# Kernel tuning notes

Hardware: AMD Instinct MI355X
Metric: run time of the kernel (lower is better)

Reference implementation:

```python
import jax, jax.numpy as jnp
import numpy as np

N = 50000   # nodes
E = 800000  # edges (before self-loops)
IN, HID, OUT = 128, 128, 64


def gcn_norm(edge_index, num_nodes):
    # add self loops with weight 1, then symmetric deg^-1/2 normalization
    loop = jnp.arange(num_nodes, dtype=edge_index.dtype)
    row = jnp.concatenate([edge_index[0], loop])
    col = jnp.concatenate([edge_index[1], loop])
    ew = jnp.ones(row.shape[0], dtype=jnp.float32)
    deg = jax.ops.segment_sum(ew, col, num_segments=num_nodes)
    dis = jnp.where(deg > 0, jax.lax.rsqrt(deg), 0.0)
    norm = dis[row] * ew * dis[col]
    return row, col, norm


def gcn_conv(x, row, col, norm, W, b):
    h = x @ W                                   # [N, F_out] dense GEMM
    msg = h[row] * norm[:, None]                # gather + scale over edges
    out = jax.ops.segment_sum(msg, col, num_segments=x.shape[0])  # scatter-add
    return out + b


def setup_inputs() -> dict:
    key = jax.random.key(0)
    k0, k1, k2, k3, k4, k5 = jax.random.split(key, 6)
    x = jax.random.normal(k0, (N, IN), dtype=jnp.float32)
    edge_index = jax.random.randint(k1, (2, E), 0, N, dtype=jnp.int32)
    # glorot-style init for linear weights, zeros for bias (PyG default)
    W1 = jax.random.normal(k2, (IN, HID), dtype=jnp.float32) * np.float32(np.sqrt(1.0 / IN))
    b1 = jnp.zeros((HID,), dtype=jnp.float32)
    W2 = jax.random.normal(k3, (HID, OUT), dtype=jnp.float32) * np.float32(np.sqrt(1.0 / HID))
    b2 = jnp.zeros((OUT,), dtype=jnp.float32)
    return {"x": x, "edge_index": edge_index, "W1": W1, "b1": b1, "W2": W2, "b2": b2}


def reference(x, edge_index, W1, b1, W2, b2):
    row, col, norm = gcn_norm(edge_index, x.shape[0])
    h = jax.nn.relu(gcn_conv(x, row, col, norm, W1, b1))
    # dropout is a no-op in eval mode (training=False)
    out = gcn_conv(h, row, col, norm, W2, b2)
    return out
```

## Files before the change

### kernel.cpp

```cpp
#include <hip/hip_runtime.h>
#include <hip/hip_fp16.h>


#define Nn 50000
#define Ne 800000
#define SCAN_B ((Nn + 1023) / 1024)

using f16x8 = _Float16 __attribute__((ext_vector_type(8)));
using f32x4 = float __attribute__((ext_vector_type(4)));

__global__ __launch_bounds__(256) void k_count(const int* __restrict__ col,
                                               int* __restrict__ degi,
                                               unsigned short* __restrict__ rank) {
  int e = blockIdx.x * 256 + threadIdx.x;
  if (e < Ne) rank[e] = (unsigned short)atomicAdd(&degi[col[e]], 1);
}

__global__ __launch_bounds__(1024) void k_scan1(const int* __restrict__ degi,
                                                int* __restrict__ rowptr,
                                                float* __restrict__ dis,
                                                int* __restrict__ bsum) {
  __shared__ int wsum[16];
  int tid = threadIdx.x;
  int lane = tid & 63, wid = tid >> 6;
  int i = blockIdx.x * 1024 + tid;
  int v = (i < Nn) ? degi[i] : 0;
  if (i < Nn) dis[i] = rsqrtf((float)(v + 1));
  int incl = v;
  #pragma unroll
  for (int off = 1; off < 64; off <<= 1) {
    int t = __shfl_up(incl, off);
    if (lane >= off) incl += t;
  }
  if (lane == 63) wsum[wid] = incl;
  __syncthreads();
  if (wid == 0) {
    int wv = (lane < 16) ? wsum[lane] : 0;
    #pragma unroll
    for (int off = 1; off < 16; off <<= 1) {
      int t = __shfl_up(wv, off);
      if (lane >= off) wv += t;
    }
    if (lane < 16) wsum[lane] = wv;
  }
  __syncthreads();
  int woff = (wid > 0) ? wsum[wid - 1] : 0;
  if (i < Nn) rowptr[i] = woff + incl - v;
  if (tid == 0) bsum[blockIdx.x] = wsum[15];
}

__global__ __launch_bounds__(1024) void k_scan3(int* __restrict__ rowptr,
                                                const int* __restrict__ bsum) {
  __shared__ int off_s;
  int tid = threadIdx.x;
  if (tid < 64) {
    int v = (tid < SCAN_B) ? bsum[tid] : 0;
    int incl = v;
    #pragma unroll
    for (int off = 1; off < 64; off <<= 1) {
      int t = __shfl_up(incl, off);
      if (tid >= off) incl += t;
    }
    if (tid == (int)blockIdx.x) off_s = incl - v;
    if (blockIdx.x == 0 && tid == SCAN_B - 1) rowptr[Nn] = incl;
  }
  __syncthreads();
  int i = blockIdx.x * 1024 + tid;
  if (i < Nn) rowptr[i] += off_s;
}

__global__ __launch_bounds__(256) void k_fill(const int* __restrict__ row,
                                              const int* __restrict__ col,
                                              const int* __restrict__ rowptr,
                                              const unsigned short* __restrict__ rank,
                                              unsigned short* __restrict__ csr) {
  int e = blockIdx.x * 256 + threadIdx.x;
  if (e >= Ne) return;
  int r = row[e], c = col[e];
  csr[rowptr[c] + (int)rank[e]] = (unsigned short)r;
}

template <int LDO>
__global__ __launch_bounds__(256) void k_gemm_mfma(const float* __restrict__ X,
                                                   const float* __restrict__ W,
                                                   __half* __restrict__ H, int n) {
  __shared__ _Float16 Xs[64 * 136];
  __shared__ _Float16 Wts[LDO * 136];
  const int tid = threadIdx.x;
  const int base = blockIdx.x * 64;

  {
    constexpr int C4 = LDO / 4;
    for (int idx4 = tid; idx4 < 32 * LDO; idx4 += 256) {
      int k = idx4 / C4;
      int c = (idx4 % C4) * 4;
      float4 wv = ((const float4*)W)[idx4];
      Wts[(c + 0) * 136 + k] = (_Float16)wv.x;
      Wts[(c + 1) * 136 + k] = (_Float16)wv.y;
      Wts[(c + 2) * 136 + k] = (_Float16)wv.z;
      Wts[(c + 3) * 136 + k] = (_Float16)wv.w;
    }
  }
  {
    for (int u = tid; u < 64 * 16; u += 256) {
      int r = u >> 4, seg = u & 15;
      int node = base + r;
      if (node >= n) node = n - 1;
      const float4* xg = (const float4*)(X + (size_t)node * 128 + seg * 8);
      float4 x0 = xg[0], x1 = xg[1];
      f16x8 hv;
      hv[0] = (_Float16)x0.x; hv[1] = (_Float16)x0.y;
      hv[2] = (_Float16)x0.z; hv[3] = (_Float16)x0.w;
      hv[4] = (_Float16)x1.x; hv[5] = (_Float16)x1.y;
      hv[6] = (_Float16)x1.z; hv[7] = (_Float16)x1.w;
      *(f16x8*)&Xs[r * 136 + seg * 8] = hv;
    }
  }
  __syncthreads();

  const int w = tid >> 6, lane = tid & 63;
  const int quad = lane >> 4, mrow = lane & 15;
  constexpr int NCT = LDO / 16;

  f32x4 acc[NCT];
  #pragma unroll
  for (int ct = 0; ct < NCT; ++ct) acc[ct] = (f32x4){0.f, 0.f, 0.f, 0.f};

  #pragma unroll
  for (int ko = 0; ko < 4; ++ko) {
    f16x8 av = *(const f16x8*)&Xs[(w * 16 + mrow) * 136 + ko * 32 + quad * 8];
    #pragma unroll
    for (int ct = 0; ct < NCT; ++ct) {
      f16x8 bv = *(const f16x8*)&Wts[(ct * 16 + mrow) * 136 + ko * 32 + quad * 8];
      acc[ct] = __builtin_amdgcn_mfma_f32_16x16x32_f16(av, bv, acc[ct], 0, 0, 0);
    }
  }

  #pragma unroll
  for (int ct = 0; ct < NCT; ++ct) {
    #pragma unroll
    for (int r = 0; r < 4; ++r) {
      int node = base + w * 16 + quad * 4 + r;
      if (node < n)
        H[(size_t)node * LDO + ct * 16 + mrow] = __float2half(acc[ct][r]);
    }
  }
}

__device__ __forceinline__ float2 h2f(unsigned int u) {
  return __half22float2(*(const __half2*)&u);
}

__global__ __launch_bounds__(256) void k_agg128_gemm64(
    const __half* __restrict__ H, const unsigned short* __restrict__ csr,
    const int* __restrict__ rowptr, const float* __restrict__ dis,
    const float* __restrict__ bias, const float* __restrict__ W2,
    __half* __restrict__ H2, int n) {
  __shared__ _Float16 Wts[64 * 136];
  __shared__ _Float16 Hs[16 * 136];

  const int tid = threadIdx.x;
  const int wid = tid >> 6, lane = tid & 63;
  const int sub = lane >> 4, fl = lane & 15;
  const int nb = wid * 4 + sub;
  const int v = blockIdx.x * 16 + nb;

  for (int idx4 = tid; idx4 < 2048; idx4 += 256) {
    int k = idx4 >> 4;
    int c = (idx4 & 15) * 4;
    float4 wv = ((const float4*)W2)[idx4];
    Wts[(c + 0) * 136 + k] = (_Float16)wv.x;
    Wts[(c + 1) * 136 + k] = (_Float16)wv.y;
    Wts[(c + 2) * 136 + k] = (_Float16)wv.z;
    Wts[(c + 3) * 136 + k] = (_Float16)wv.w;
  }

  float a0 = 0, a1 = 0, a2 = 0, a3 = 0, a4 = 0, a5 = 0, a6 = 0, a7 = 0;
  float d = 0.f;
  if (v < n) {
    int s = rowptr[v], e = rowptr[v + 1];
    d = dis[v];
    float sw = d * d;
    const uint4* Hq = (const uint4*)H;
    uint4 hv = Hq[(size_t)v * 16 + fl];
    float2 p0 = h2f(hv.x), p1 = h2f(hv.y), p2 = h2f(hv.z), p3 = h2f(hv.w);
    a0 = p0.x * sw; a1 = p0.y * sw; a2 = p1.x * sw; a3 = p1.y * sw;
    a4 = p2.x * sw; a5 = p2.y * sw; a6 = p3.x * sw; a7 = p3.y * sw;
    constexpr int D = 6;
    int i = s;
    for (; i + D <= e; i += D) {
      int srcs[D];
      uint4 q[D];
      float wd[D];
      #pragma unroll
      for (int j = 0; j < D; ++j) srcs[j] = csr[i + j];
      #pragma unroll
      for (int j = 0; j < D; ++j) q[j] = Hq[(size_t)srcs[j] * 16 + fl];
      #pragma unroll
      for (int j = 0; j < D; ++j) wd[j] = dis[srcs[j]];
      #pragma unroll
      for (int j = 0; j < D; ++j) {
        float w = wd[j] * d;
        float2 t;
        t = h2f(q[j].x); a0 = fmaf(w, t.x, a0); a1 = fmaf(w, t.y, a1);
        t = h2f(q[j].y); a2 = fmaf(w, t.x, a2); a3 = fmaf(w, t.y, a3);
        t = h2f(q[j].z); a4 = fmaf(w, t.x, a4); a5 = fmaf(w, t.y, a5);
        t = h2f(q[j].w); a6 = fmaf(w, t.x, a6); a7 = fmaf(w, t.y, a7);
      }
    }
    if (i < e) {
      int srcs[D];
      uint4 q[D];
      float wd[D];
      #pragma unroll
      for (int j = 0; j < D; ++j) {
        int idx = (i + j < e) ? i + j : e - 1;
        srcs[j] = csr[idx];
      }
      #pragma unroll
      for (int j = 0; j < D; ++j) q[j] = Hq[(size_t)srcs[j] * 16 + fl];
      #pragma unroll
      for (int j = 0; j < D; ++j) wd[j] = dis[srcs[j]];
      #pragma unroll
      for (int j = 0; j < D; ++j) {
        float w = (i + j < e) ? wd[j] * d : 0.f;
        float2 t;
        t = h2f(q[j].x); a0 = fmaf(w, t.x, a0); a1 = fmaf(w, t.y, a1);
        t = h2f(q[j].y); a2 = fmaf(w, t.x, a2); a3 = fmaf(w, t.y, a3);
        t = h2f(q[j].z); a4 = fmaf(w, t.x, a4); a5 = fmaf(w, t.y, a5);
        t = h2f(q[j].w); a6 = fmaf(w, t.x, a6); a7 = fmaf(w, t.y, a7);
      }
    }
  }
  {
    const float4* Bq = (const float4*)bias;
    float4 b0 = Bq[fl * 2], b1v = Bq[fl * 2 + 1];
    f16x8 hrow;
    hrow[0] = (_Float16)fmaxf(a0 + b0.x, 0.f);
    hrow[1] = (_Float16)fmaxf(a1 + b0.y, 0.f);
    hrow[2] = (_Float16)fmaxf(a2 + b0.z, 0.f);
    hrow[3] = (_Float16)fmaxf(a3 + b0.w, 0.f);
    hrow[4] = (_Float16)fmaxf(a4 + b1v.x, 0.f);
    hrow[5] = (_Float16)fmaxf(a5 + b1v.y, 0.f);
    hrow[6] = (_Float16)fmaxf(a6 + b1v.z, 0.f);
    hrow[7] = (_Float16)fmaxf(a7 + b1v.w, 0.f);
    *(f16x8*)&Hs[nb * 136 + fl * 8] = hrow;
  }
  __syncthreads();

  const int quad = lane >> 4, mrow = lane & 15;
  f32x4 acc = (f32x4){0.f, 0.f, 0.f, 0.f};
  #pragma unroll
  for (int ko = 0; ko < 4; ++ko) {
    f16x8 av = *(const f16x8*)&Hs[mrow * 136 + ko * 32 + quad * 8];
    f16x8 bv = *(const f16x8*)&Wts[(wid * 16 + mrow) * 136 + ko * 32 + quad * 8];
    acc = __builtin_amdgcn_mfma_f32_16x16x32_f16(av, bv, acc, 0, 0, 0);
  }
  #pragma unroll
  for (int r = 0; r < 4; ++r) {
    int node = blockIdx.x * 16 + quad * 4 + r;
    if (node < n)
      H2[(size_t)node * 64 + wid * 16 + mrow] = __float2half(acc[r]);
  }
}

__global__ __launch_bounds__(256) void k_agg64(const __half* __restrict__ H,
                                               const unsigned short* __restrict__ csr,
                                               const int* __restrict__ rowptr,
                                               const float* __restrict__ dis,
                                               const float* __restrict__ bias,
                                               float* __restrict__ Out, int n) {
  const int wid = threadIdx.x >> 6, lane = threadIdx.x & 63;
  const int sub = lane >> 4, fl = lane & 15;
  int v = blockIdx.x * 16 + wid * 4 + sub;
  if (v >= n) return;
  int s = rowptr[v], e = rowptr[v + 1];
  float d = dis[v];
  float sw = d * d;
  const uint2* Hq = (const uint2*)H;
  uint2 hv = Hq[(size_t)v * 16 + fl];
  float2 p0 = h2f(hv.x), p1 = h2f(hv.y);
  float a0 = p0.x * sw, a1 = p0.y * sw, a2 = p1.x * sw, a3 = p1.y * sw;
  constexpr int D = 8;
  int i = s;
  for (; i + D <= e; i += D) {
    int srcs[D];
    uint2 q[D];
    float wd[D];
    #pragma unroll
    for (int j = 0; j < D; ++j) srcs[j] = csr[i + j];
    #pragma unroll
    for (int j = 0; j < D; ++j) q[j] = Hq[(size_t)srcs[j] * 16 + fl];
    #pragma unroll
    for (int j = 0; j < D; ++j) wd[j] = dis[srcs[j]];
    #pragma unroll
    for (int j = 0; j < D; ++j) {
      float w = wd[j] * d;
      float2 t;
      t = h2f(q[j].x); a0 = fmaf(w, t.x, a0); a1 = fmaf(w, t.y, a1);
      t = h2f(q[j].y); a2 = fmaf(w, t.x, a2); a3 = fmaf(w, t.y, a3);
    }
  }
  if (i < e) {
    int srcs[D];
    uint2 q[D];
    float wd[D];
    #pragma unroll
    for (int j = 0; j < D; ++j) {
      int idx = (i + j < e) ? i + j : e - 1;
      srcs[j] = csr[idx];
    }
    #pragma unroll
    for (int j = 0; j < D; ++j) q[j] = Hq[(size_t)srcs[j] * 16 + fl];
    #pragma unroll
    for (int j = 0; j < D; ++j) wd[j] = dis[srcs[j]];
    #pragma unroll
    for (int j = 0; j < D; ++j) {
      float w = (i + j < e) ? wd[j] * d : 0.f;
      float2 t;
      t = h2f(q[j].x); a0 = fmaf(w, t.x, a0); a1 = fmaf(w, t.y, a1);
      t = h2f(q[j].y); a2 = fmaf(w, t.x, a2); a3 = fmaf(w, t.y, a3);
    }
  }
  const float4* Bq = (const float4*)bias;
  float4 b = Bq[fl];
  float4 o = make_float4(a0 + b.x, a1 + b.y, a2 + b.z, a3 + b.w);
  ((float4*)(Out + (size_t)v * 64))[fl] = o;
}

extern "C" void kernel_launch(void* const* d_in, const int* in_sizes, int n_in,
                              void* d_out, int out_size, void* d_ws, size_t ws_size,
                              hipStream_t stream) {
  const float* x  = (const float*)d_in[0];
  const int*   ei = (const int*)d_in[1];
  const int*   row = ei;
  const int*   col = ei + Ne;
  const float* W1 = (const float*)d_in[2];
  const float* b1 = (const float*)d_in[3];
  const float* W2 = (const float*)d_in[4];
  const float* b2 = (const float*)d_in[5];
  float* out = (float*)d_out;

  char* ws = (char*)d_ws;
  size_t off = 0;
  auto alloc = [&](size_t bytes) -> void* {
    void* p = ws + off;
    off += (bytes + 255) & ~(size_t)255;
    return p;
  };
  int*    degi   = (int*)   alloc(Nn * sizeof(int));
  int*    rowptr = (int*)   alloc((Nn + 1) * sizeof(int));
  float*  dis    = (float*) alloc(Nn * sizeof(float));
  int*    bsum   = (int*)   alloc(64 * sizeof(int));
  unsigned short* rank = (unsigned short*)alloc((size_t)Ne * sizeof(unsigned short));
  unsigned short* csr  = (unsigned short*)alloc((size_t)Ne * sizeof(unsigned short));
  __half* H1     = (__half*)alloc((size_t)Nn * 128 * sizeof(__half));
  __half* H2     = (__half*)alloc((size_t)Nn * 64 * sizeof(__half));

  hipMemsetAsync(degi, 0, Nn * sizeof(int), stream);

  const int EB  = (Ne + 255) / 256;
  const int NGB = (Nn + 15) / 16;
  const int GT  = (Nn + 63) / 64;

  k_count<<<EB, 256, 0, stream>>>(col, degi, rank);
  k_scan1<<<SCAN_B, 1024, 0, stream>>>(degi, rowptr, dis, bsum);
  k_scan3<<<SCAN_B, 1024, 0, stream>>>(rowptr, bsum);
  k_fill<<<EB, 256, 0, stream>>>(row, col, rowptr, rank, csr);

  k_gemm_mfma<128><<<GT, 256, 0, stream>>>(x, W1, H1, Nn);
  k_agg128_gemm64<<<NGB, 256, 0, stream>>>(H1, csr, rowptr, dis, b1, W2, H2, Nn);
  k_agg64<<<NGB, 256, 0, stream>>>(H2, csr, rowptr, dis, b2, out, Nn);
}
```

Measured before the change: 207.5 us.

## Sort nodes by degree for load-balanced aggregation and vectorize edge preprocessing

Builds a degree histogram during the scan, prefix-sums it, and produces a permutation that groups nodes of equal degree. Both aggregation kernels then process nodes in that order, so the 16-lane groups and wavefronts handle nodes with similar edge counts and diverge less. The count and fill kernels also process two edges per thread using int2/ushort2 loads. This adds two small kernels plus an atomic-based permutation, and the aggregation's neighbour accesses become less local because consecutive blocks now touch scattered nodes.

```diff
diff --git a/kernel.cpp b/kernel.cpp
--- a/kernel.cpp
+++ b/kernel.cpp
@@ -5,27 +5,41 @@
 #define Nn 50000
 #define Ne 800000
 #define SCAN_B ((Nn + 1023) / 1024)
+#define NBUCK 512
 
 using f16x8 = _Float16 __attribute__((ext_vector_type(8)));
 using f32x4 = float __attribute__((ext_vector_type(4)));
 
-__global__ __launch_bounds__(256) void k_count(const int* __restrict__ col,
+__global__ __launch_bounds__(256) void k_count(const int2* __restrict__ col2,
                                                int* __restrict__ degi,
-                                               unsigned short* __restrict__ rank) {
-  int e = blockIdx.x * 256 + threadIdx.x;
-  if (e < Ne) rank[e] = (unsigned short)atomicAdd(&degi[col[e]], 1);
+                                               ushort2* __restrict__ rank2) {
+  int t = blockIdx.x * 256 + threadIdx.x;
+  if (t < Ne / 2) {
+    int2 c = col2[t];
+    unsigned short r0 = (unsigned short)atomicAdd(&degi[c.x], 1);
+    unsigned short r1 = (unsigned short)atomicAdd(&degi[c.y], 1);
+    ushort2 rk; rk.x = r0; rk.y = r1;
+    rank2[t] = rk;
+  }
 }
 
 __global__ __launch_bounds__(1024) void k_scan1(const int* __restrict__ degi,
                                                 int* __restrict__ rowptr,
                                                 float* __restrict__ dis,
-                                                int* __restrict__ bsum) {
+                                                int* __restrict__ bsum,
+                                                int* __restrict__ dhist) {
   __shared__ int wsum[16];
+  __shared__ int lh[NBUCK];
   int tid = threadIdx.x;
   int lane = tid & 63, wid = tid >> 6;
+  if (tid < NBUCK) lh[tid] = 0;
+  __syncthreads();
   int i = blockIdx.x * 1024 + tid;
   int v = (i < Nn) ? degi[i] : 0;
-  if (i < Nn) dis[i] = rsqrtf((float)(v + 1));
+  if (i < Nn) {
+    dis[i] = rsqrtf((float)(v + 1));
+    atomicAdd(&lh[v < NBUCK ? v : NBUCK - 1], 1);
+  }
   int incl = v;
   #pragma unroll
   for (int off = 1; off < 64; off <<= 1) {
@@ -47,6 +61,7 @@
   int woff = (wid > 0) ? wsum[wid - 1] : 0;
   if (i < Nn) rowptr[i] = woff + incl - v;
   if (tid == 0) bsum[blockIdx.x] = wsum[15];
+  if (tid < NBUCK && lh[tid]) atomicAdd(&dhist[tid], lh[tid]);
 }
 
 __global__ __launch_bounds__(1024) void k_scan3(int* __restrict__ rowptr,
@@ -69,15 +84,56 @@
   if (i < Nn) rowptr[i] += off_s;
 }
 
-__global__ __launch_bounds__(256) void k_fill(const int* __restrict__ row,
-                                              const int* __restrict__ col,
+__global__ __launch_bounds__(512) void k_dscan(const int* __restrict__ dhist,
+                                               int* __restrict__ doff) {
+  __shared__ int ws[8];
+  int tid = threadIdx.x, lane = tid & 63, wid = tid >> 6;
+  int v = dhist[tid];
+  int incl = v;
+  #pragma unroll
+  for (int off = 1; off < 64; off <<= 1) {
+    int t = __shfl_up(incl, off);
+    if (lane >= off) incl += t;
+  }
+  if (lane == 63) ws[wid] = incl;
+  __syncthreads();
+  if (wid == 0) {
+    int wv = (lane < 8) ? ws[lane] : 0;
+    #pragma unroll
+    for (int off = 1; off < 8; off <<= 1) {
+      int t = __shfl_up(wv, off);
+      if (lane >= off) wv += t;
+    }
+    if (lane < 8) ws[lane] = wv;
+  }
+  __syncthreads();
+  int woff = (wid > 0) ? ws[wid - 1] : 0;
+  doff[tid] = woff + incl - v;
+}
+
+__global__ __launch_bounds__(256) void k_perm(const int* __restrict__ degi,
+                                              int* __restrict__ doff,
+                                              int* __restrict__ perm) {
+  int i = blockIdx.x * 256 + threadIdx.x;
+  if (i < Nn) {
+    int d = degi[i]; if (d >= NBUCK) d = NBUCK - 1;
+    int pos = atomicAdd(&doff[d], 1);
+    perm[pos] = i;
+  }
+}
+
+__global__ __launch_bounds__(256) void k_fill(const int2* __restrict__ row2,
+                                              const int2* __restrict__ col2,
                                               const int* __restrict__ rowptr,
-                                              const unsigned short* __restrict__ rank,
+                                              const ushort2* __restrict__ rank2,
                                               unsigned short* __restrict__ csr) {
-  int e = blockIdx.x * 256 + threadIdx.x;
-  if (e >= Ne) return;
-  int r = row[e], c = col[e];
-  csr[rowptr[c] + (int)rank[e]] = (unsigned short)r;
+  int t = blockIdx.x * 256 + threadIdx.x;
+  if (t >= Ne / 2) return;
+  int2 r = row2[t];
+  int2 c = col2[t];
+  ushort2 k = rank2[t];
+  csr[rowptr[c.x] + (int)k.x] = (unsigned short)r.x;
+  csr[rowptr[c.y] + (int)k.y] = (unsigned short)r.y;
 }
 
 template <int LDO>
@@ -154,16 +210,19 @@
 __global__ __launch_bounds__(256) void k_agg128_gemm64(
     const __half* __restrict__ H, const unsigned short* __restrict__ csr,
     const int* __restrict__ rowptr, const float* __restrict__ dis,
+    const int* __restrict__ perm,
     const float* __restrict__ bias, const float* __restrict__ W2,
     __half* __restrict__ H2, int n) {
   __shared__ _Float16 Wts[64 * 136];
   __shared__ _Float16 Hs[16 * 136];
+  __shared__ int spv[16];
 
   const int tid = threadIdx.x;
   const int wid = tid >> 6, lane = tid & 63;
   const int sub = lane >> 4, fl = lane & 15;
   const int nb = wid * 4 + sub;
-  const int v = blockIdx.x * 16 + nb;
+  const int v = perm[blockIdx.x * 16 + nb];
+  if (fl == 0) spv[nb] = v;
 
   for (int idx4 = tid; idx4 < 2048; idx4 += 256) {
     int k = idx4 >> 4;
@@ -175,61 +234,57 @@
     Wts[(c + 3) * 136 + k] = (_Float16)wv.w;
   }
 
-  float a0 = 0, a1 = 0, a2 = 0, a3 = 0, a4 = 0, a5 = 0, a6 = 0, a7 = 0;
-  float d = 0.f;
-  if (v < n) {
-    int s = rowptr[v], e = rowptr[v + 1];
-    d = dis[v];
-    float sw = d * d;
-    const uint4* Hq = (const uint4*)H;
-    uint4 hv = Hq[(size_t)v * 16 + fl];
-    float2 p0 = h2f(hv.x), p1 = h2f(hv.y), p2 = h2f(hv.z), p3 = h2f(hv.w);
-    a0 = p0.x * sw; a1 = p0.y * sw; a2 = p1.x * sw; a3 = p1.y * sw;
-    a4 = p2.x * sw; a5 = p2.y * sw; a6 = p3.x * sw; a7 = p3.y * sw;
-    constexpr int D = 6;
-    int i = s;
-    for (; i + D <= e; i += D) {
-      int srcs[D];
-      uint4 q[D];
-      float wd[D];
-      #pragma unroll
-      for (int j = 0; j < D; ++j) srcs[j] = csr[i + j];
-      #pragma unroll
-      for (int j = 0; j < D; ++j) q[j] = Hq[(size_t)srcs[j] * 16 + fl];
-      #pragma unroll
-      for (int j = 0; j < D; ++j) wd[j] = dis[srcs[j]];
-      #pragma unroll
-      for (int j = 0; j < D; ++j) {
-        float w = wd[j] * d;
-        float2 t;
-        t = h2f(q[j].x); a0 = fmaf(w, t.x, a0); a1 = fmaf(w, t.y, a1);
-        t = h2f(q[j].y); a2 = fmaf(w, t.x, a2); a3 = fmaf(w, t.y, a3);
-        t = h2f(q[j].z); a4 = fmaf(w, t.x, a4); a5 = fmaf(w, t.y, a5);
-        t = h2f(q[j].w); a6 = fmaf(w, t.x, a6); a7 = fmaf(w, t.y, a7);
-      }
-    }
-    if (i < e) {
-      int srcs[D];
-      uint4 q[D];
-      float wd[D];
-      #pragma unroll
-      for (int j = 0; j < D; ++j) {
-        int idx = (i + j < e) ? i + j : e - 1;
-        srcs[j] = csr[idx];
-      }
-      #pragma unroll
-      for (int j = 0; j < D; ++j) q[j] = Hq[(size_t)srcs[j] * 16 + fl];
-      #pragma unroll
-      for (int j = 0; j < D; ++j) wd[j] = dis[srcs[j]];
-      #pragma unroll
-      for (int j = 0; j < D; ++j) {
-        float w = (i + j < e) ? wd[j] * d : 0.f;
-        float2 t;
-        t = h2f(q[j].x); a0 = fmaf(w, t.x, a0); a1 = fmaf(w, t.y, a1);
-        t = h2f(q[j].y); a2 = fmaf(w, t.x, a2); a3 = fmaf(w, t.y, a3);
-        t = h2f(q[j].z); a4 = fmaf(w, t.x, a4); a5 = fmaf(w, t.y, a5);
-        t = h2f(q[j].w); a6 = fmaf(w, t.x, a6); a7 = fmaf(w, t.y, a7);
-      }
+  int s = rowptr[v], e = rowptr[v + 1];
+  float d = dis[v];
+  float sw = d * d;
+  const uint4* Hq = (const uint4*)H;
+  uint4 hv = Hq[(size_t)v * 16 + fl];
+  float2 p0 = h2f(hv.x), p1 = h2f(hv.y), p2 = h2f(hv.z), p3 = h2f(hv.w);
+  float a0 = p0.x * sw, a1 = p0.y * sw, a2 = p1.x * sw, a3 = p1.y * sw;
+  float a4 = p2.x * sw, a5 = p2.y * sw, a6 = p3.x * sw, a7 = p3.y * sw;
+  constexpr int D = 6;
+  int i = s;
+  for (; i + D <= e; i += D) {
+    int srcs[D];
+    uint4 q[D];
+    float wd[D];
+    #pragma unroll
+    for (int j = 0; j < D; ++j) srcs[j] = csr[i + j];
+    #pragma unroll
+    for (int j = 0; j < D; ++j) q[j] = Hq[(size_t)srcs[j] * 16 + fl];
+    #pragma unroll
+    for (int j = 0; j < D; ++j) wd[j] = dis[srcs[j]];
+    #pragma unroll
+    for (int j = 0; j < D; ++j) {
+      float w = wd[j] * d;
+      float2 t;
+      t = h2f(q[j].x); a0 = fmaf(w, t.x, a0); a1 = fmaf(w, t.y, a1);
+      t = h2f(q[j].y); a2 = fmaf(w, t.x, a2); a3 = fmaf(w, t.y, a3);
+      t = h2f(q[j].z); a4 = fmaf(w, t.x, a4); a5 = fmaf(w, t.y, a5);
+      t = h2f(q[j].w); a6 = fmaf(w, t.x, a6); a7 = fmaf(w, t.y, a7);
+    }
+  }
+  if (i < e) {
+    int srcs[D];
+    uint4 q[D];
+    float wd[D];
+    #pragma unroll
+    for (int j = 0; j < D; ++j) {
+      int idx = (i + j < e) ? i + j : e - 1;
+      srcs[j] = csr[idx];
+    }
+    #pragma unroll
+    for (int j = 0; j < D; ++j) q[j] = Hq[(size_t)srcs[j] * 16 + fl];
+    #pragma unroll
+    for (int j = 0; j < D; ++j) wd[j] = dis[srcs[j]];
+    #pragma unroll
+    for (int j = 0; j < D; ++j) {
+      float w = (i + j < e) ? wd[j] * d : 0.f;
+      float2 t;
+      t = h2f(q[j].x); a0 = fmaf(w, t.x, a0); a1 = fmaf(w, t.y, a1);
+      t = h2f(q[j].y); a2 = fmaf(w, t.x, a2); a3 = fmaf(w, t.y, a3);
+      t = h2f(q[j].z); a4 = fmaf(w, t.x, a4); a5 = fmaf(w, t.y, a5);
+      t = h2f(q[j].w); a6 = fmaf(w, t.x, a6); a7 = fmaf(w, t.y, a7);
     }
   }
   {
@@ -258,9 +313,8 @@
   }
   #pragma unroll
   for (int r = 0; r < 4; ++r) {
-    int node = blockIdx.x * 16 + quad * 4 + r;
-    if (node < n)
-      H2[(size_t)node * 64 + wid * 16 + mrow] = __float2half(acc[r]);
+    int node = spv[quad * 4 + r];
+    H2[(size_t)node * 64 + wid * 16 + mrow] = __float2half(acc[r]);
   }
 }
 
@@ -268,12 +322,12 @@
                                                const unsigned short* __restrict__ csr,
                                                const int* __restrict__ rowptr,
                                                const float* __restrict__ dis,
+                                               const int* __restrict__ perm,
                                                const float* __restrict__ bias,
                                                float* __restrict__ Out, int n) {
   const int wid = threadIdx.x >> 6, lane = threadIdx.x & 63;
   const int sub = lane >> 4, fl = lane & 15;
-  int v = blockIdx.x * 16 + wid * 4 + sub;
-  if (v >= n) return;
+  int v = perm[blockIdx.x * 16 + wid * 4 + sub];
   int s = rowptr[v], e = rowptr[v + 1];
   float d = dis[v];
   float sw = d * d;
@@ -349,26 +403,32 @@
     return p;
   };
   int*    degi   = (int*)   alloc(Nn * sizeof(int));
+  int*    dhist  = (int*)   alloc(NBUCK * sizeof(int));
+  int*    doff   = (int*)   alloc(NBUCK * sizeof(int));
   int*    rowptr = (int*)   alloc((Nn + 1) * sizeof(int));
   float*  dis    = (float*) alloc(Nn * sizeof(float));
   int*    bsum   = (int*)   alloc(64 * sizeof(int));
+  int*    perm   = (int*)   alloc(Nn * sizeof(int));
   unsigned short* rank = (unsigned short*)alloc((size_t)Ne * sizeof(unsigned short));
   unsigned short* csr  = (unsigned short*)alloc((size_t)Ne * sizeof(unsigned short));
   __half* H1     = (__half*)alloc((size_t)Nn * 128 * sizeof(__half));
   __half* H2     = (__half*)alloc((size_t)Nn * 64 * sizeof(__half));
 
-  hipMemsetAsync(degi, 0, Nn * sizeof(int), stream);
-
-  const int EB  = (Ne + 255) / 256;
+  hipMemsetAsync(degi, 0, ((Nn * sizeof(int) + 255) & ~(size_t)255) + NBUCK * sizeof(int), stream);
+
+  const int E2B = (Ne / 2 + 255) / 256;
   const int NGB = (Nn + 15) / 16;
   const int GT  = (Nn + 63) / 64;
 
-  k_count<<<EB, 256, 0, stream>>>(col, degi, rank);
-  k_scan1<<<SCAN_B, 1024, 0, stream>>>(degi, rowptr, dis, bsum);
+  k_count<<<E2B, 256, 0, stream>>>((const int2*)col, degi, (ushort2*)rank);
+  k_scan1<<<SCAN_B, 1024, 0, stream>>>(degi, rowptr, dis, bsum, dhist);
   k_scan3<<<SCAN_B, 1024, 0, stream>>>(rowptr, bsum);
-  k_fill<<<EB, 256, 0, stream>>>(row, col, rowptr, rank, csr);
+  k_dscan<<<1, 512, 0, stream>>>(dhist, doff);
+  k_perm<<<(Nn + 255) / 256, 256, 0, stream>>>(degi, doff, perm);
+  k_fill<<<E2B, 256, 0, stream>>>((const int2*)row, (const int2*)col, rowptr,
+                                  (const ushort2*)rank, csr);
 
   k_gemm_mfma<128><<<GT, 256, 0, stream>>>(x, W1, H1, Nn);
-  k_agg128_gemm64<<<NGB, 256, 0, stream>>>(H1, csr, rowptr, dis, b1, W2, H2, Nn);
-  k_agg64<<<NGB, 256, 0, stream>>>(H2, csr, rowptr, dis, b2, out, Nn);
-}
+  k_agg128_gemm64<<<NGB, 256, 0, stream>>>(H1, csr, rowptr, dis, perm, b1, W2, H2, Nn);
+  k_agg64<<<NGB, 256, 0, stream>>>(H2, csr, rowptr, dis, perm, b2, out, Nn);
+}
```

After: 339.9 us. 1.64x slower.
